# Kernel tuning notes

Measured on AMD Instinct MI355X. Metric: run time of the kernel, lower is better.

The kernel has to match this reference:

```python
import jax, jax.numpy as jnp
import numpy as np

B, L, H, NH = 2, 256, 512, 8
DH = H // NH
MAXLEN = 256           # module's max_seq_len; pe index offset
PE_ROWS = 2 * MAXLEN + 1


def _lin(x, W, b):
    # torch nn.Linear convention: y = x @ W.T + b
    return x @ W.T + b


def setup_inputs() -> dict:
    rng = jax.random.key(0)
    ks = jax.random.split(rng, 24)
    s = 0.02
    inp = {
        "key": jax.random.normal(ks[0], (B, L, H), jnp.float32),
        "query": jax.random.normal(ks[1], (B, L, H), jnp.float32),
        "value": jax.random.normal(ks[2], (B, L, H), jnp.float32),
        # learned params
        "pe": jax.random.normal(ks[3], (PE_ROWS, H), jnp.float32) * s,
        "Wf": jax.random.normal(ks[4], (H, 4 * H), jnp.float32) * s,
        "bf": jnp.zeros((H,), jnp.float32),
        "Wk": jax.random.normal(ks[5], (H, H), jnp.float32) * s,
        "bk": jnp.zeros((H,), jnp.float32),
        "Wq": jax.random.normal(ks[6], (H, H), jnp.float32) * s,
        "bq": jnp.zeros((H,), jnp.float32),
        "Wv": jax.random.normal(ks[7], (H, H), jnp.float32) * s,
        "bv": jnp.zeros((H,), jnp.float32),
        "Wr": jax.random.normal(ks[8], (H, H), jnp.float32) * s,
        "br": jnp.zeros((H,), jnp.float32),
        "Wo": jax.random.normal(ks[9], (H, H), jnp.float32) * s,  # ff_final
        "bo": jnp.zeros((H,), jnp.float32),
        "u": jax.random.normal(ks[10], (NH, DH), jnp.float32) * s,
        "v": jax.random.normal(ks[11], (NH, DH), jnp.float32) * s,
        # int inputs
        "seq_len": jax.random.randint(ks[12], (B,), 100, 200).astype(jnp.int64),
        "lex_num": jax.random.randint(ks[13], (B,), 0, 50).astype(jnp.int64),
    }
    pos_s = jax.random.randint(ks[14], (B, L), 0, 250)
    pos_e = pos_s + jax.random.randint(ks[15], (B, L), 0, 5)
    inp["pos_s"] = pos_s.astype(jnp.int64)
    inp["pos_e"] = pos_e.astype(jnp.int64)
    return inp


def reference(key, query, value, pe, Wf, bf, Wk, bk, Wq, bq, Wv, bv, Wr, br,
              Wo, bo, u, v, seq_len, lex_num, pos_s, pos_e):
    b, l, _ = key.shape
    # four relative position matrices [B, L, L]
    pos_ss = pos_s[:, :, None] - pos_s[:, None, :]
    pos_se = pos_s[:, :, None] - pos_e[:, None, :]
    pos_es = pos_e[:, :, None] - pos_s[:, None, :]
    pos_ee = pos_e[:, :, None] - pos_e[:, None, :]
    # gather pe embeddings, each [B, L, L, H]
    pe_ss = pe[pos_ss + MAXLEN]
    pe_se = pe[pos_se + MAXLEN]
    pe_es = pe[pos_es + MAXLEN]
    pe_ee = pe[pos_ee + MAXLEN]
    pe_4 = jnp.concatenate([pe_ss, pe_se, pe_es, pe_ee], axis=-1)  # [B,L,L,4H]
    rel = jax.nn.relu(_lin(pe_4, Wf, bf))                          # 'ff' fusion -> [B,L,L,H]

    q = _lin(query, Wq, bq).reshape(b, l, NH, DH).transpose(0, 2, 1, 3)  # [B,nh,L,dh]
    k = _lin(key, Wk, bk).reshape(b, l, NH, DH).transpose(0, 2, 1, 3)
    val = _lin(value, Wv, bv).reshape(b, l, NH, DH).transpose(0, 2, 1, 3)
    rel = _lin(rel, Wr, br).reshape(b, l, l, NH, DH)               # [B,L,L,nh,dh]

    A = jnp.einsum('bhid,bhjd->bhij', q, k)
    B_ = jnp.einsum('bhid,bijhd->bhij', q, rel)
    C = jnp.einsum('hd,bhjd->bhj', u, k)[:, :, None, :]
    D = jnp.einsum('hd,bijhd->bhij', v, rel)

    score = (A + B_ + C + D) / np.float32(np.sqrt(DH))
    total_len = seq_len + lex_num                                   # [B]
    mask = (jnp.arange(l)[None, :] < total_len[:, None])[:, None, None, :]
    score = jnp.where(mask, score, jnp.float32(-1e15))
    attn = jax.nn.softmax(score, axis=-1)
    out = jnp.einsum('bhij,bhjd->bhid', attn, val)                  # [B,nh,L,dh]
    out = out.transpose(0, 2, 1, 3).reshape(b, l, H)
    return _lin(out, Wo, bo)
```

## Files before the change

### kernel.cpp

```cpp
#include <hip/hip_runtime.h>
#include <hip/hip_bf16.h>

typedef unsigned short USHORT;
typedef long long LL;
typedef short s8v __attribute__((ext_vector_type(8)));
typedef float f32x4 __attribute__((ext_vector_type(4)));


__device__ __forceinline__ float bf2f(USHORT u) {
  union { unsigned int i; float f; } v; v.i = ((unsigned int)u) << 16; return v.f;
}
__device__ __forceinline__ USHORT f2bf(float f) {
  unsigned int x = __float_as_uint(f);
  return (USHORT)((x + 0x7fffu + ((x >> 16) & 1u)) >> 16);
}

struct PrepArgs {
  const void* fsrc[18]; USHORT* fdst[18]; int fn[18];
  const void* wr_src; USHORT* wrT;
  const void* isrc[4]; int* idst[4];
};

__global__ __launch_bounds__(256) void prep_k(PrepArgs a, const void* qraw, int* flags) {
  __shared__ int s_w;
  const int t = threadIdx.x;
  if (t == 0) s_w = 0;
  __syncthreads();
  const USHORT* qb = (const USHORT*)qraw;
  int wild = 0;
  for (int c = t; c < 512; c += 256) {
    float x = bf2f(qb[c]);
    if (!(fabsf(x) <= 1024.0f)) wild = 1;
  }
  if (wild) atomicAdd(&s_w, 1);
  __syncthreads();
  const int f = (s_w == 0) ? 1 : 0;

  const int y = blockIdx.y;
  if (y < 18) {
    const int n = a.fn[y];
    const USHORT* sb = (const USHORT*)a.fsrc[y];
    const float* sf = (const float*)a.fsrc[y];
    USHORT* d = a.fdst[y];
    for (int idx = blockIdx.x * 256 + t; idx < n; idx += gridDim.x * 256)
      d[idx] = f ? sb[idx] : f2bf(sf[idx]);
  } else if (y == 18) {
    const USHORT* sb = (const USHORT*)a.wr_src;
    const float* sf = (const float*)a.wr_src;
    for (int idx = blockIdx.x * 256 + t; idx < 262144; idx += gridDim.x * 256) {
      const int e = idx >> 9, dd = idx & 511;
      const int s = dd * 512 + e;
      a.wrT[idx] = f ? sb[s] : f2bf(sf[s]);
    }
  } else if (blockIdx.x == 0) {
    if (t == 0) flags[0] = f;
    const int fi = (((const int*)a.isrc[0])[1] == 0) ? 1 : 0;
    if (t < 2) {
      a.idst[0][t] = fi ? (int)((const LL*)a.isrc[0])[t] : ((const int*)a.isrc[0])[t];
      a.idst[1][t] = fi ? (int)((const LL*)a.isrc[1])[t] : ((const int*)a.isrc[1])[t];
    }
    for (int c = t; c < 512; c += 256) {
      a.idst[2][c] = fi ? (int)((const LL*)a.isrc[2])[c] : ((const int*)a.isrc[2])[c];
      a.idst[3][c] = fi ? (int)((const LL*)a.isrc[3])[c] : ((const int*)a.isrc[3])[c];
    }
  }
}

struct GDesc {
  const USHORT* A; const USHORT* W; const USHORT* bias;
  void* out;
  int M, N, K, lda, ldw, koff, ldo, mode, trans, pad;
};
struct GArgs { GDesc d[32]; };

__global__ __launch_bounds__(256) void gemm2_k(GArgs ga, const int* __restrict__ flags) {
  const GDesc de = ga.d[blockIdx.z];
  const int row0 = blockIdx.y * 64, col0 = blockIdx.x * 64;
  if (row0 >= de.M || col0 >= de.N) return;
  const int wave = threadIdx.x >> 6, lane = threadIdx.x & 63;
  const int mrow = row0 + wave * 16 + (lane & 15);
  const int kq = (lane >> 4) * 8;
  const bool mok = (mrow < de.M);
  const USHORT* ar = de.A + (long)(mok ? mrow : row0) * de.lda + kq;
  const int nc = col0 + (lane & 15);
  const USHORT* w0p = de.W + (long)(nc +  0) * de.ldw + de.koff + kq;
  const USHORT* w1p = de.W + (long)(nc + 16) * de.ldw + de.koff + kq;
  const USHORT* w2p = de.W + (long)(nc + 32) * de.ldw + de.koff + kq;
  const USHORT* w3p = de.W + (long)(nc + 48) * de.ldw + de.koff + kq;

  f32x4 acc[4] = {};
#pragma unroll 4
  for (int k0 = 0; k0 < de.K; k0 += 32) {
    s8v a = *(const s8v*)(ar + k0);
    s8v wv0 = *(const s8v*)(w0p + k0);
    s8v wv1 = *(const s8v*)(w1p + k0);
    s8v wv2 = *(const s8v*)(w2p + k0);
    s8v wv3 = *(const s8v*)(w3p + k0);
    acc[0] = __builtin_amdgcn_mfma_f32_16x16x32_bf16(a, wv0, acc[0], 0, 0, 0);
    acc[1] = __builtin_amdgcn_mfma_f32_16x16x32_bf16(a, wv1, acc[1], 0, 0, 0);
    acc[2] = __builtin_amdgcn_mfma_f32_16x16x32_bf16(a, wv2, acc[2], 0, 0, 0);
    acc[3] = __builtin_amdgcn_mfma_f32_16x16x32_bf16(a, wv3, acc[3], 0, 0, 0);
  }

  const int obf = (de.mode == 2) ? flags[0] : (de.mode == 1);
  const int mbase = row0 + wave * 16 + (lane >> 4) * 4;
#pragma unroll
  for (int nt = 0; nt < 4; nt++) {
    const int n = col0 + nt * 16 + (lane & 15);
    const float bias = de.bias ? bf2f(de.bias[n]) : 0.f;
#pragma unroll
    for (int r = 0; r < 4; r++) {
      const int m = mbase + r;
      if (m >= de.M) continue;
      const float vo = acc[nt][r] + bias;
      const long off = de.trans ? ((long)n * de.ldo + m) : ((long)m * de.ldo + n);
      if (obf) ((USHORT*)de.out)[off] = f2bf(vo);
      else     ((float*)de.out)[off] = vo;
    }
  }
}

__global__ __launch_bounds__(256) void mid_k(
    const USHORT* __restrict__ Ptab, const USHORT* __restrict__ q_n,
    const USHORT* __restrict__ k_n, const USHORT* __restrict__ WrT,
    const USHORT* __restrict__ u_bf, const USHORT* __restrict__ v_bf,
    const USHORT* __restrict__ br_bf,
    USHORT* __restrict__ P12, USHORT* __restrict__ P34,
    float* __restrict__ cbv, float* __restrict__ uk, USHORT* __restrict__ vwr)
{
  const int bid = blockIdx.x, t = threadIdx.x, gsz = gridDim.x;
  const long TS = 513l * 512;
  for (int r = bid; r < 5130; r += gsz) {
    const int half = (r >= 2565) ? 1 : 0;
    const int rr = half ? (r - 2565) : r;
    const int S0 = rr / 5, dj = rr % 5;
    const USHORT* pa = Ptab + (half ? 2 * TS : 0) + (long)S0 * 512;
    const USHORT* pb = Ptab + (half ? 3 * TS : TS) + (long)max(S0 - dj, 0) * 512;
    USHORT* to = (half ? P34 : P12) + (long)rr * 512;
    const int e = t * 2;
    ushort2 xa = *(const ushort2*)(pa + e);
    ushort2 xb = *(const ushort2*)(pb + e);
    ushort2 o;
    o.x = f2bf(bf2f(xa.x) + bf2f(xb.x));
    o.y = f2bf(bf2f(xa.y) + bf2f(xb.y));
    *(ushort2*)(to + e) = o;
  }
  for (int idx = bid * 256 + t; idx < 262144; idx += gsz * 256) {
    const int hd = idx & 511;
    float s = (bf2f(q_n[idx]) + bf2f(v_bf[hd])) * bf2f(br_bf[hd]);
    float s2 = bf2f(k_n[idx]) * bf2f(u_bf[hd]);
#pragma unroll
    for (int off = 32; off > 0; off >>= 1) { s += __shfl_xor(s, off); s2 += __shfl_xor(s2, off); }
    if ((t & 63) == 0) { cbv[idx >> 6] = s; uk[idx >> 6] = s2; }
  }
  for (int o = bid * 256 + t; o < 4096; o += gsz * 256) {
    const int h = o >> 9, e = o & 511;
    float s = 0.f;
    const USHORT* wrow = WrT + (long)e * 512 + h * 64;
    const USHORT* vrow = v_bf + h * 64;
#pragma unroll
    for (int d = 0; d < 64; d += 4) {
      ushort4 wv = *(const ushort4*)(wrow + d);
      ushort4 vv = *(const ushort4*)(vrow + d);
      s += bf2f(vv.x) * bf2f(wv.x) + bf2f(vv.y) * bf2f(wv.y) +
           bf2f(vv.z) * bf2f(wv.z) + bf2f(vv.w) * bf2f(wv.w);
    }
    vwr[o] = f2bf(s);
  }
}

__global__ __launch_bounds__(128) void score4_k(
    const USHORT* __restrict__ P12, const USHORT* __restrict__ P34,
    const float* __restrict__ cbv, const float* __restrict__ uk,
    const USHORT* __restrict__ wbuf,
    const int* __restrict__ seq_len, const int* __restrict__ lex_num,
    const int* __restrict__ pos_s, const int* __restrict__ pos_e,
    float* __restrict__ S)
{
  const int i = blockIdx.x, b = blockIdx.y;
  const int wave = threadIdx.x >> 6, lane = threadIdx.x & 63;
  const int jt = blockIdx.z * 2 + wave;
  int tl = seq_len[b] + lex_num[b];
  tl = min(max(tl, 1), 256);
  const int j0 = jt * 16;
  if (j0 >= tl) return;
  const int n = lane & 15, q = lane >> 4;
  const int psi = pos_s[b * 256 + i], pei = pos_e[b * 256 + i];
  const int j = j0 + n;
  const int psj = pos_s[b * 256 + j], pej = pos_e[b * 256 + j];
  const int S0 = min(max(psi - psj + 256, 0), 512);
  const int di = min(max(pei - psi, 0), 4);
  const int dj = min(max(pej - psj, 0), 4);
  const USHORT* p12 = P12 + ((long)(S0 * 5 + dj)) * 512 + q * 8;
  const USHORT* p34 = P34 + ((long)(min(S0 + di, 512) * 5 + dj)) * 512 + q * 8;
  const USHORT* wr = wbuf + ((long)((b * 8 + (n & 7)) * 256 + i)) * 512 + q * 8;

  f32x4 acc = {0.f, 0.f, 0.f, 0.f};
#pragma unroll
  for (int kk = 0; kk < 16; kk++) {
    s8v xa = *(const s8v*)(p12 + kk * 32);
    s8v xb = *(const s8v*)(p34 + kk * 32);
    s8v wv = *(const s8v*)(wr + kk * 32);
    s8v af;
#pragma unroll
    for (int x = 0; x < 8; x++) {
      float fs = bf2f((USHORT)xa[x]) + bf2f((USHORT)xb[x]);
      fs = fmaxf(fs, 0.f);
      af[x] = (short)(USHORT)((__float_as_uint(fs) + 0x8000u) >> 16);
    }
    acc = __builtin_amdgcn_mfma_f32_16x16x32_bf16(af, wv, acc, 0, 0, 0);
  }
  if (n < 8) {
    const long base = (long)(b * 8 + n) * 256 + i;
    const float cb = cbv[(long)(b * 256 + i) * 8 + n];
    float* dst = S + base * 256 + j0 + q * 4;
    const float4 sac = *(const float4*)dst;
    const float* sacp = (const float*)&sac;
#pragma unroll
    for (int r = 0; r < 4; r++) {
      const int jr = j0 + q * 4 + r;
      dst[r] = (acc[r] + sacp[r] + cb + uk[(long)(b * 256 + jr) * 8 + n]) * 0.125f;
    }
  }
}

__global__ __launch_bounds__(256) void softav_k(
    const float* __restrict__ S, const USHORT* __restrict__ v_t,
    const int* __restrict__ seq_len, const int* __restrict__ lex_num,
    USHORT* __restrict__ out_pre)
{
  __shared__ float att[8 * 256];
  __shared__ float red4[4];
  const int i = blockIdx.x, b = blockIdx.y, t = threadIdx.x;
  const int lane = t & 63, wave = t >> 6;
  int tl = seq_len[b] + lex_num[b];
  tl = min(max(tl, 1), 256);
  for (int h = 0; h < 8; h++) {
    const long base = ((long)(b * 8 + h) * 256 + i) * 256;
    const float val = (t < tl) ? S[base + t] : -3.0e38f;
    float m = val;
#pragma unroll
    for (int off = 32; off > 0; off >>= 1) m = fmaxf(m, __shfl_xor(m, off));
    if (lane == 0) red4[wave] = m;
    __syncthreads();
    m = fmaxf(fmaxf(red4[0], red4[1]), fmaxf(red4[2], red4[3]));
    const float pv = (t < tl) ? __expf(val - m) : 0.f;
    float s = pv;
#pragma unroll
    for (int off = 32; off > 0; off >>= 1) s += __shfl_xor(s, off);
    __syncthreads();
    if (lane == 0) red4[wave] = s;
    __syncthreads();
    s = red4[0] + red4[1] + red4[2] + red4[3];
    if (!(s > 1e-30f)) s = 1.f;
    att[h * 256 + t] = pv / s;
    __syncthreads();
  }
#pragma unroll
  for (int pass = 0; pass < 2; pass++) {
    const int h = (t >> 6) + 4 * pass;
    const int d = t & 63;
    const USHORT* vrow = v_t + (long)(h * 64 + d) * 512 + b * 256;
    const float* arow = &att[h * 256];
    float acc = 0.f;
    const int tl4 = (tl + 3) & ~3;
    for (int jj = 0; jj < tl4; jj += 4) {
      ushort4 vv = *(const ushort4*)(vrow + jj);
      acc += arow[jj + 0] * bf2f(vv.x) + arow[jj + 1] * bf2f(vv.y) +
             arow[jj + 2] * bf2f(vv.z) + arow[jj + 3] * bf2f(vv.w);
    }
    out_pre[(long)(b * 256 + i) * 512 + h * 64 + d] = f2bf(acc);
  }
}

extern "C" void kernel_launch(void* const* d_in, const int* in_sizes, int n_in,
                              void* d_out, int out_size, void* d_ws, size_t ws_size,
                              hipStream_t stream) {
  (void)in_sizes; (void)n_in; (void)out_size; (void)ws_size;

  char* w = (char*)d_ws;
  auto take = [&](size_t n) { char* r = w; w += (n + 255) & ~(size_t)255; return r; };

  int* flags   = (int*)take(16);
  int* c_seq   = (int*)take(16);
  int* c_lex   = (int*)take(16);
  int* c_pos_s = (int*)take(2048);
  int* c_pos_e = (int*)take(2048);
  const int ns[18] = {262144,262144,262144,262656,1048576,512,262144,512,262144,512,
                      262144,512,262144,512,262144,512,512,512};
  USHORT* canon[18];
  for (int i = 0; i < 18; i++) canon[i] = (USHORT*)take((size_t)ns[i] * 2);
  USHORT* WrT     = (USHORT*)take((size_t)262144 * 2);
  USHORT* q_n     = (USHORT*)take((size_t)262144 * 2);
  USHORT* k_n     = (USHORT*)take((size_t)262144 * 2);
  USHORT* v_t     = (USHORT*)take((size_t)262144 * 2);
  USHORT* wbuf    = (USHORT*)take((size_t)2097152 * 2);
  USHORT* Ptab    = (USHORT*)take((size_t)1050624 * 2);
  USHORT* P12     = (USHORT*)take((size_t)2565 * 512 * 2);
  USHORT* P34     = (USHORT*)take((size_t)2565 * 512 * 2);
  USHORT* vwr     = (USHORT*)take((size_t)4096 * 2);
  USHORT* out_pre = (USHORT*)take((size_t)262144 * 2);
  float* S   = (float*)take((size_t)1048576 * 4);
  float* cbv = (float*)take((size_t)4096 * 4);
  float* uk  = (float*)take((size_t)4096 * 4);

  PrepArgs pa;
  for (int i = 0; i < 18; i++) { pa.fsrc[i] = d_in[i]; pa.fdst[i] = canon[i]; pa.fn[i] = ns[i]; }
  pa.wr_src = d_in[12]; pa.wrT = WrT;
  for (int i = 0; i < 4; i++) pa.isrc[i] = d_in[18 + i];
  pa.idst[0] = c_seq; pa.idst[1] = c_lex; pa.idst[2] = c_pos_s; pa.idst[3] = c_pos_e;
  prep_k<<<dim3(64, 20), 256, 0, stream>>>(pa, d_in[1], flags);

  GArgs gA = {};
  for (int z = 0; z < 4; z++)
    gA.d[z] = {canon[3], canon[4], (z == 0) ? canon[5] : nullptr, Ptab + (long)z * 513 * 512,
               513, 512, 512, 512, 2048, z * 512, 512, 1, 0, 0};
  gA.d[4] = {canon[1], canon[8],  canon[9],  q_n, 512, 512, 512, 512, 512, 0, 512, 1, 0, 0};
  gA.d[5] = {canon[0], canon[6],  canon[7],  k_n, 512, 512, 512, 512, 512, 0, 512, 1, 0, 0};
  gA.d[6] = {canon[2], canon[10], canon[11], v_t, 512, 512, 512, 512, 512, 0, 512, 1, 1, 0};
  gemm2_k<<<dim3(8, 9, 7), 256, 0, stream>>>(gA, flags);

  mid_k<<<512, 256, 0, stream>>>(Ptab, q_n, k_n, WrT, canon[16], canon[17], canon[13],
                                 P12, P34, cbv, uk, vwr);

  GArgs gB = {};
  for (int z = 0; z < 16; z++) {
    const int b = z >> 3, h = z & 7;
    gB.d[z] = {q_n + b * 131072 + h * 64, WrT, vwr + h * 512, wbuf + (long)z * 131072,
               256, 512, 64, 512, 512, h * 64, 512, 1, 0, 0};
  }
  for (int z = 0; z < 16; z++) {
    const int b = z >> 3, h = z & 7;
    gB.d[16 + z] = {q_n + b * 131072 + h * 64, k_n + b * 131072 + h * 64, nullptr,
                    S + (long)z * 65536, 256, 256, 64, 512, 512, 0, 256, 0, 0, 0};
  }
  gemm2_k<<<dim3(8, 4, 32), 256, 0, stream>>>(gB, flags);

  score4_k<<<dim3(256, 2, 8), 128, 0, stream>>>(
      P12, P34, cbv, uk, wbuf, c_seq, c_lex, c_pos_s, c_pos_e, S);

  softav_k<<<dim3(256, 2), 256, 0, stream>>>(S, v_t, c_seq, c_lex, out_pre);

  GArgs gC = {};
  gC.d[0] = {out_pre, canon[14], canon[15], d_out, 512, 512, 512, 512, 512, 0, 512, 2, 0, 0};
  gemm2_k<<<dim3(8, 8, 1), 256, 0, stream>>>(gC, flags);
}
```

Measured before the change: 226.6 us.

## Precompute full relu'd relative-position table per (S0,di,dj) and simplify score kernel

Result: no change. 223.2 us (-1.5%).

```diff
diff --git a/kernel.cpp b/kernel.cpp
--- a/kernel.cpp
+++ b/kernel.cpp
@@ -125,24 +125,26 @@
     const USHORT* __restrict__ k_n, const USHORT* __restrict__ WrT,
     const USHORT* __restrict__ u_bf, const USHORT* __restrict__ v_bf,
     const USHORT* __restrict__ br_bf,
-    USHORT* __restrict__ P12, USHORT* __restrict__ P34,
+    USHORT* __restrict__ T,
     float* __restrict__ cbv, float* __restrict__ uk, USHORT* __restrict__ vwr)
 {
   const int bid = blockIdx.x, t = threadIdx.x, gsz = gridDim.x;
   const long TS = 513l * 512;
-  for (int r = bid; r < 5130; r += gsz) {
-    const int half = (r >= 2565) ? 1 : 0;
-    const int rr = half ? (r - 2565) : r;
-    const int S0 = rr / 5, dj = rr % 5;
-    const USHORT* pa = Ptab + (half ? 2 * TS : 0) + (long)S0 * 512;
-    const USHORT* pb = Ptab + (half ? 3 * TS : TS) + (long)max(S0 - dj, 0) * 512;
-    USHORT* to = (half ? P34 : P12) + (long)rr * 512;
+  for (int r = bid; r < 12825; r += gsz) {
+    const int S0 = r / 25, rem = r % 25, di = rem / 5, dj = rem % 5;
+    const USHORT* p1 = Ptab + (long)S0 * 512;
+    const USHORT* p2 = Ptab + TS + (long)max(S0 - dj, 0) * 512;
+    const USHORT* p3 = Ptab + 2 * TS + (long)min(S0 + di, 512) * 512;
+    const USHORT* p4 = Ptab + 3 * TS + (long)min(max(S0 + di - dj, 0), 512) * 512;
+    USHORT* to = T + (long)r * 512;
     const int e = t * 2;
-    ushort2 xa = *(const ushort2*)(pa + e);
-    ushort2 xb = *(const ushort2*)(pb + e);
+    ushort2 x1 = *(const ushort2*)(p1 + e);
+    ushort2 x2 = *(const ushort2*)(p2 + e);
+    ushort2 x3 = *(const ushort2*)(p3 + e);
+    ushort2 x4 = *(const ushort2*)(p4 + e);
     ushort2 o;
-    o.x = f2bf(bf2f(xa.x) + bf2f(xb.x));
-    o.y = f2bf(bf2f(xa.y) + bf2f(xb.y));
+    o.x = f2bf(fmaxf(bf2f(x1.x) + bf2f(x2.x) + bf2f(x3.x) + bf2f(x4.x), 0.f));
+    o.y = f2bf(fmaxf(bf2f(x1.y) + bf2f(x2.y) + bf2f(x3.y) + bf2f(x4.y), 0.f));
     *(ushort2*)(to + e) = o;
   }
   for (int idx = bid * 256 + t; idx < 262144; idx += gsz * 256) {
@@ -169,8 +171,8 @@
   }
 }
 
-__global__ __launch_bounds__(128) void score4_k(
-    const USHORT* __restrict__ P12, const USHORT* __restrict__ P34,
+__global__ __launch_bounds__(256) void score5_k(
+    const USHORT* __restrict__ T,
     const float* __restrict__ cbv, const float* __restrict__ uk,
     const USHORT* __restrict__ wbuf,
     const int* __restrict__ seq_len, const int* __restrict__ lex_num,
@@ -179,7 +181,7 @@
 {
   const int i = blockIdx.x, b = blockIdx.y;
   const int wave = threadIdx.x >> 6, lane = threadIdx.x & 63;
-  const int jt = blockIdx.z * 2 + wave;
+  const int jt = blockIdx.z * 4 + wave;
   int tl = seq_len[b] + lex_num[b];
   tl = min(max(tl, 1), 256);
   const int j0 = jt * 16;
@@ -191,24 +193,15 @@
   const int S0 = min(max(psi - psj + 256, 0), 512);
   const int di = min(max(pei - psi, 0), 4);
   const int dj = min(max(pej - psj, 0), 4);
-  const USHORT* p12 = P12 + ((long)(S0 * 5 + dj)) * 512 + q * 8;
-  const USHORT* p34 = P34 + ((long)(min(S0 + di, 512) * 5 + dj)) * 512 + q * 8;
+  const USHORT* tp = T + ((long)(S0 * 25 + di * 5 + dj)) * 512 + q * 8;
   const USHORT* wr = wbuf + ((long)((b * 8 + (n & 7)) * 256 + i)) * 512 + q * 8;
 
   f32x4 acc = {0.f, 0.f, 0.f, 0.f};
 #pragma unroll
   for (int kk = 0; kk < 16; kk++) {
-    s8v xa = *(const s8v*)(p12 + kk * 32);
-    s8v xb = *(const s8v*)(p34 + kk * 32);
+    s8v av = *(const s8v*)(tp + kk * 32);
     s8v wv = *(const s8v*)(wr + kk * 32);
-    s8v af;
-#pragma unroll
-    for (int x = 0; x < 8; x++) {
-      float fs = bf2f((USHORT)xa[x]) + bf2f((USHORT)xb[x]);
-      fs = fmaxf(fs, 0.f);
-      af[x] = (short)(USHORT)((__float_as_uint(fs) + 0x8000u) >> 16);
-    }
-    acc = __builtin_amdgcn_mfma_f32_16x16x32_bf16(af, wv, acc, 0, 0, 0);
+    acc = __builtin_amdgcn_mfma_f32_16x16x32_bf16(av, wv, acc, 0, 0, 0);
   }
   if (n < 8) {
     const long base = (long)(b * 8 + n) * 256 + i;
@@ -296,8 +289,7 @@
   USHORT* v_t     = (USHORT*)take((size_t)262144 * 2);
   USHORT* wbuf    = (USHORT*)take((size_t)2097152 * 2);
   USHORT* Ptab    = (USHORT*)take((size_t)1050624 * 2);
-  USHORT* P12     = (USHORT*)take((size_t)2565 * 512 * 2);
-  USHORT* P34     = (USHORT*)take((size_t)2565 * 512 * 2);
+  USHORT* T       = (USHORT*)take((size_t)12825 * 512 * 2);
   USHORT* vwr     = (USHORT*)take((size_t)4096 * 2);
   USHORT* out_pre = (USHORT*)take((size_t)262144 * 2);
   float* S   = (float*)take((size_t)1048576 * 4);
@@ -321,7 +313,7 @@
   gemm2_k<<<dim3(8, 9, 7), 256, 0, stream>>>(gA, flags);
 
   mid_k<<<512, 256, 0, stream>>>(Ptab, q_n, k_n, WrT, canon[16], canon[17], canon[13],
-                                 P12, P34, cbv, uk, vwr);
+                                 T, cbv, uk, vwr);
 
   GArgs gB = {};
   for (int z = 0; z < 16; z++) {
@@ -336,8 +328,8 @@
   }
   gemm2_k<<<dim3(8, 4, 32), 256, 0, stream>>>(gB, flags);
 
-  score4_k<<<dim3(256, 2, 8), 128, 0, stream>>>(
-      P12, P34, cbv, uk, wbuf, c_seq, c_lex, c_pos_s, c_pos_e, S);
+  score5_k<<<dim3(256, 2, 4), 256, 0, stream>>>(
+      T, cbv, uk, wbuf, c_seq, c_lex, c_pos_s, c_pos_e, S);
 
   softav_k<<<dim3(256, 2), 256, 0, stream>>>(S, v_t, c_seq, c_lex, out_pre);
 
```
